# Kernel tuning notes

Measured on AMD Instinct MI355X. Metric: run time of the kernel, lower is better.

The kernel has to match this reference:

```python
import jax, jax.numpy as jnp
import numpy as np

NEG_SLOPE = 0.01   # F.leaky_relu default
EPS_NORM = 1e-12   # F.normalize default eps

N_NODES = 20000
N_RAND_EDGES = 320000
D_IN = 128
D_EMB = 128
C1 = 256
C2 = 32


def _segment_mean(vals, idx, n):
    s = jax.ops.segment_sum(vals, idx, num_segments=n)
    cnt = jax.ops.segment_sum(jnp.ones((vals.shape[0],), vals.dtype), idx, num_segments=n)
    return s / jnp.maximum(cnt, 1.0)[:, None]


def gcn_mean_sparse(h, W, b, src, dst, n):
    # GCN_layer with att=False: copy_u + mean over in-neighbors
    z = h @ W + b
    return _segment_mean(z[src], dst, n)


def gat_sparse(h, W, b, aW, ab, src, dst, n):
    # GCN_layer with att=True on an edge-list graph.
    # att_linear(cat(src,dst)) decomposed: e = leaky_relu(z_src@aWs + z_dst@aWd + ab)
    z = h @ W + b                       # [n, c]
    c = z.shape[-1]
    a_src = (z @ aW[:c])[:, 0]          # [n]
    a_dst = (z @ aW[c:])[:, 0]          # [n]
    e = jax.nn.leaky_relu(a_src[src] + a_dst[dst] + ab[0], NEG_SLOPE)  # [E]
    m = jax.ops.segment_max(e, dst, num_segments=n)                    # softmax over mailbox (per dst)
    alpha = jnp.exp(e - m[dst])
    denom = jax.ops.segment_sum(alpha, dst, num_segments=n)
    num = jax.ops.segment_sum(alpha[:, None] * z[src], dst, num_segments=n)  # [n, c]
    return num / denom[:, None]


def gat_dense(h, W, b, aW, ab):
    # att=True on a complete graph (coarse levels): dense softmax over src axis per dst
    z = h @ W + b                       # [n, c]
    c = z.shape[-1]
    a_src = z @ aW[:c]                  # [n, 1]
    a_dst = z @ aW[c:]                  # [n, 1]
    e = jax.nn.leaky_relu(a_src + a_dst.T + ab[0], NEG_SLOPE)  # [n_src, n_dst]
    alpha = jax.nn.softmax(e, axis=0)
    return jnp.einsum('ij,ic->jc', alpha, z)


def setup_inputs() -> dict:
    key = jax.random.key(0)
    ks = jax.random.split(key, 16)
    feature = jax.random.normal(ks[0], (N_NODES, D_IN), dtype=jnp.float32)
    src = jax.random.randint(ks[1], (N_RAND_EDGES,), 0, N_NODES, dtype=jnp.int32)
    dst = jax.random.randint(ks[2], (N_RAND_EDGES,), 0, N_NODES, dtype=jnp.int32)
    loop = jnp.arange(N_NODES, dtype=jnp.int32)
    edge_index = jnp.stack([jnp.concatenate([src, loop]), jnp.concatenate([dst, loop])])

    def lin(k, fan_in, fan_out):
        s = 1.0 / np.sqrt(fan_in)
        kw, kb = jax.random.split(k)
        W = jax.random.uniform(kw, (fan_in, fan_out), jnp.float32, -s, s)
        b = jax.random.uniform(kb, (fan_out,), jnp.float32, -s, s)
        return W, b

    Wf, bf = lin(ks[3], D_IN, D_EMB)          # GCN_f1
    We1, be1 = lin(ks[4], D_EMB, D_EMB)       # assign layer 1: GCN_emb
    Wa1, ba1 = lin(ks[5], D_EMB, C1)          # assign layer 1: GCN_ass linear
    attW1, attb1 = lin(ks[6], 2 * C1, 1)      # assign layer 1: att_linear
    We2, be2 = lin(ks[7], D_EMB, D_EMB)       # assign layer 2: GCN_emb
    Wa2, ba2 = lin(ks[8], D_EMB, C2)          # assign layer 2: GCN_ass linear
    attW2, attb2 = lin(ks[9], 2 * C2, 1)      # assign layer 2: att_linear
    return dict(feature=feature, edge_index=edge_index,
                Wf=Wf, bf=bf, We1=We1, be1=be1, Wa1=Wa1, ba1=ba1,
                attW1=attW1, attb1=attb1, We2=We2, be2=be2, Wa2=Wa2,
                ba2=ba2, attW2=attW2, attb2=attb2)


def reference(feature, edge_index, Wf, bf, We1, be1, Wa1, ba1, attW1, attb1,
              We2, be2, Wa2, ba2, attW2, attb2):
    src, dst = edge_index[0], edge_index[1]
    n = feature.shape[0]
    # GCN_f1 (att=False) + L2 normalize
    x = gcn_mean_sparse(feature, Wf, bf, src, dst, n)
    x = x / jnp.maximum(jnp.linalg.norm(x, axis=-1, keepdims=True), EPS_NORM)
    embed3 = x                                           # tree_node_embed[3]
    # Assign layer 1 (on original sparse graph)
    z1 = gcn_mean_sparse(x, We1, be1, src, dst, n)       # GCN_emb
    s1 = jax.nn.softmax(gat_sparse(z1, Wa1, ba1, attW1, attb1, src, dst, n), axis=-1)
    x1 = s1.T @ z1                                       # tree_node_embed[2], [C1, D]
    # Coarse graph: s^T A s with strictly positive softmax s -> complete graph
    # (setdiag(0) then add_self_loop => all pairs incl. self loops)
    # Assign layer 2 (dense complete graph over C1 nodes)
    lin2 = x1 @ We2 + be2
    z2 = jnp.broadcast_to(jnp.mean(lin2, axis=0, keepdims=True), lin2.shape)  # mean over all in-neighbors
    s2 = jax.nn.softmax(gat_dense(z2, Wa2, ba2, attW2, attb2), axis=-1)
    x2 = s2.T @ z2                                       # tree_node_embed[1], [C2, D]
    embed0 = jnp.mean(x2)                                # tree_node_embed[0] (scalar mean of all elems)
    assign1 = jnp.ones((s2.shape[-1], 1), dtype=x2.dtype)  # assignmatrix[1]
    # (assignmatrix[3], assignmatrix[2], assignmatrix[1], embed[3], embed[2], embed[1], embed[0])
    return (s1, s2, assign1, embed3, x1, x2, embed0)
```

## Files before the change

### kernel.cpp

```cpp
#include <hip/hip_runtime.h>
#include <hip/hip_bf16.h>
#include <math.h>

#define NN 20000
#define DD 128
#define CC1 256
#define CC2 32
#define X1_SPLIT 128

__device__ __forceinline__ unsigned short f2bf(float f) {
    unsigned int b = __float_as_uint(f);
    b = (b + 0x7fffu + ((b >> 16) & 1u)) >> 16;
    return (unsigned short)b;
}
__device__ __forceinline__ float bf_lo(unsigned int u) { return __uint_as_float(u << 16); }
__device__ __forceinline__ float bf_hi(unsigned int u) { return __uint_as_float(u & 0xffff0000u); }

__global__ void k_count(const int* __restrict__ dst, int* __restrict__ cnt, int E) {
    int e = blockIdx.x * blockDim.x + threadIdx.x;
    if (e < E) atomicAdd(&cnt[dst[e]], 1);
}

__global__ void k_scan(const int* __restrict__ cnt, int* __restrict__ offs, int n) {
    __shared__ int part[1024];
    int t = threadIdx.x;
    int chunk = (n + 1023) / 1024;
    int lo = t * chunk, hi = min(lo + chunk, n);
    int s = 0;
    for (int i = lo; i < hi; i++) s += cnt[i];
    part[t] = s;
    __syncthreads();
    for (int d = 1; d < 1024; d <<= 1) {
        int v = (t >= d) ? part[t - d] : 0;
        __syncthreads();
        part[t] += v;
        __syncthreads();
    }
    int base = (t > 0) ? part[t - 1] : 0;
    for (int i = lo; i < hi; i++) { offs[i] = base; base += cnt[i]; }
    if (t == 1023) offs[n] = part[1023];
}

__global__ void k_fill(const int* __restrict__ src, const int* __restrict__ dst,
                       const int* __restrict__ offs, int* __restrict__ fill,
                       int* __restrict__ csr_src, int E) {
    int e = blockIdx.x * blockDim.x + threadIdx.x;
    if (e < E) {
        int d = dst[e];
        int pos = atomicAdd(&fill[d], 1);
        csr_src[offs[d] + pos] = src[e];
    }
}

__global__ void k_fold(const float* __restrict__ Wa1, const float* __restrict__ ba1,
                       const float* __restrict__ attW1, const float* __restrict__ attb1,
                       float* __restrict__ fold) {
    int t = threadIdx.x;
    float vs = 0.f, vd = 0.f;
    for (int k = 0; k < CC1; k++) {
        float w = Wa1[t * CC1 + k];
        vs += w * attW1[k];
        vd += w * attW1[CC1 + k];
    }
    fold[t] = vs;
    fold[128 + t] = vd;
    if (t == 0) {
        float c = attb1[0];
        for (int k = 0; k < CC1; k++) c += ba1[k] * (attW1[k] + attW1[CC1 + k]);
        fold[256] = c;
    }
}

__global__ __launch_bounds__(256) void k_seg_mean(const float* __restrict__ in,
                                                  const int* __restrict__ offs,
                                                  const int* __restrict__ csr_src,
                                                  float* __restrict__ out, int n) {
    int wave = (blockIdx.x * blockDim.x + threadIdx.x) >> 6;
    int lane = threadIdx.x & 63;
    if (wave >= n) return;
    int lo = offs[wave], hi = offs[wave + 1];
    int half = lane >> 5, l32 = lane & 31;
    const float4* f4 = (const float4*)in;
    float4 acc = make_float4(0.f, 0.f, 0.f, 0.f);
    int i = lo + half;
    int sN = (i < hi) ? csr_src[i] : 0;
    while (i < hi) {
        int s = sN;
        int nx = i + 2;
        if (nx < hi) sN = csr_src[nx];
        float4 v = f4[(size_t)s * 32 + l32];
        acc.x += v.x; acc.y += v.y; acc.z += v.z; acc.w += v.w;
        i = nx;
    }
    acc.x += __shfl_xor(acc.x, 32);
    acc.y += __shfl_xor(acc.y, 32);
    acc.z += __shfl_xor(acc.z, 32);
    acc.w += __shfl_xor(acc.w, 32);
    if (half == 0) {
        float inv = 1.0f / (float)max(hi - lo, 1);
        float4 r = make_float4(acc.x * inv, acc.y * inv, acc.z * inv, acc.w * inv);
        ((float4*)out)[(size_t)wave * 32 + l32] = r;
    }
}

template <int MODE>
__global__ __launch_bounds__(256) void k_gemm128(const float* __restrict__ in,
                                                 const float* __restrict__ W,
                                                 const float* __restrict__ b,
                                                 float* __restrict__ out,
                                                 const float* __restrict__ fold,
                                                 float* __restrict__ a_src,
                                                 float* __restrict__ a_dst,
                                                 int n, int rows_per_block) {
    __shared__ float sW[128 * 128];
    __shared__ float sT[128][32];
    int t = threadIdx.x;
    for (int i = t; i < 128 * 128; i += 256) sW[i] = W[i];
    int lane = t & 63;
    int wv = t >> 6;
    int j4 = (lane & 31) * 4;
    int rh = lane >> 5;
    int rg = wv * 2 + rh;
    float bj0 = b[j4], bj1 = b[j4 + 1], bj2 = b[j4 + 2], bj3 = b[j4 + 3];
    float vs0 = 0.f, vs1 = 0.f, vs2 = 0.f, vs3 = 0.f;
    float vd0 = 0.f, vd1 = 0.f, vd2 = 0.f, vd3 = 0.f;
    if (MODE == 1) {
        vs0 = fold[j4]; vs1 = fold[j4 + 1]; vs2 = fold[j4 + 2]; vs3 = fold[j4 + 3];
        vd0 = fold[128 + j4]; vd1 = fold[128 + j4 + 1]; vd2 = fold[128 + j4 + 2]; vd3 = fold[128 + j4 + 3];
    }
    int row0 = blockIdx.x * rows_per_block;
    int row_end = min(row0 + rows_per_block, n);
    for (int r = row0; r < row_end; r += 32) {
        int nr = min(32, row_end - r);
        __syncthreads();
        {
            int lrow = t >> 3, seg = t & 7;
            if (lrow < nr) {
                const float4* g = (const float4*)&in[(size_t)(r + lrow) * 128 + seg * 16];
                float4 v0 = g[0], v1 = g[1], v2 = g[2], v3 = g[3];
                int k0 = seg * 16;
                sT[k0 + 0][lrow] = v0.x; sT[k0 + 1][lrow] = v0.y; sT[k0 + 2][lrow] = v0.z; sT[k0 + 3][lrow] = v0.w;
                sT[k0 + 4][lrow] = v1.x; sT[k0 + 5][lrow] = v1.y; sT[k0 + 6][lrow] = v1.z; sT[k0 + 7][lrow] = v1.w;
                sT[k0 + 8][lrow] = v2.x; sT[k0 + 9][lrow] = v2.y; sT[k0 + 10][lrow] = v2.z; sT[k0 + 11][lrow] = v2.w;
                sT[k0 + 12][lrow] = v3.x; sT[k0 + 13][lrow] = v3.y; sT[k0 + 14][lrow] = v3.z; sT[k0 + 15][lrow] = v3.w;
            }
        }
        __syncthreads();
        float acc[4][4];
        #pragma unroll
        for (int p = 0; p < 4; p++) { acc[p][0] = bj0; acc[p][1] = bj1; acc[p][2] = bj2; acc[p][3] = bj3; }
        for (int k = 0; k < 128; k++) {
            float4 w4 = *(const float4*)&sW[k * 128 + j4];
            float4 rv = *(const float4*)&sT[k][rg * 4];
            acc[0][0] += rv.x * w4.x; acc[0][1] += rv.x * w4.y; acc[0][2] += rv.x * w4.z; acc[0][3] += rv.x * w4.w;
            acc[1][0] += rv.y * w4.x; acc[1][1] += rv.y * w4.y; acc[1][2] += rv.y * w4.z; acc[1][3] += rv.y * w4.w;
            acc[2][0] += rv.z * w4.x; acc[2][1] += rv.z * w4.y; acc[2][2] += rv.z * w4.z; acc[2][3] += rv.z * w4.w;
            acc[3][0] += rv.w * w4.x; acc[3][1] += rv.w * w4.y; acc[3][2] += rv.w * w4.z; acc[3][3] += rv.w * w4.w;
        }
        #pragma unroll
        for (int p = 0; p < 4; p++) {
            int row = r + rg * 4 + p;
            if (MODE == 0) {
                float ss_ = acc[p][0] * acc[p][0] + acc[p][1] * acc[p][1] +
                            acc[p][2] * acc[p][2] + acc[p][3] * acc[p][3];
                ss_ += __shfl_xor(ss_, 16); ss_ += __shfl_xor(ss_, 8);
                ss_ += __shfl_xor(ss_, 4);  ss_ += __shfl_xor(ss_, 2); ss_ += __shfl_xor(ss_, 1);
                if (row < row_end) {
                    float scale = 1.0f / fmaxf(sqrtf(ss_), 1e-12f);
                    float4 o = make_float4(acc[p][0] * scale, acc[p][1] * scale, acc[p][2] * scale, acc[p][3] * scale);
                    *(float4*)&out[(size_t)row * 128 + j4] = o;
                }
            } else {
                if (row < row_end) {
                    float4 o = make_float4(acc[p][0], acc[p][1], acc[p][2], acc[p][3]);
                    *(float4*)&out[(size_t)row * 128 + j4] = o;
                }
                float ps = acc[p][0] * vs0 + acc[p][1] * vs1 + acc[p][2] * vs2 + acc[p][3] * vs3;
                float pd = acc[p][0] * vd0 + acc[p][1] * vd1 + acc[p][2] * vd2 + acc[p][3] * vd3;
                ps += __shfl_xor(ps, 16); ps += __shfl_xor(ps, 8); ps += __shfl_xor(ps, 4);
                ps += __shfl_xor(ps, 2);  ps += __shfl_xor(ps, 1);
                pd += __shfl_xor(pd, 16); pd += __shfl_xor(pd, 8); pd += __shfl_xor(pd, 4);
                pd += __shfl_xor(pd, 2);  pd += __shfl_xor(pd, 1);
                if (row < row_end && (lane & 31) == 0) {
                    a_src[row] = ps;
                    a_dst[row] = pd;
                }
            }
        }
    }
}

__global__ __launch_bounds__(256) void k_att(const float* __restrict__ z1,
                                             const int* __restrict__ offs,
                                             const int* __restrict__ csr_src,
                                             const float* __restrict__ a_src,
                                             const float* __restrict__ a_dst,
                                             const float* __restrict__ fold,
                                             float* __restrict__ r, int n) {
    int wave = (blockIdx.x * blockDim.x + threadIdx.x) >> 6;
    int lane = threadIdx.x & 63;
    if (wave >= n) return;
    int lo = offs[wave], hi = offs[wave + 1];
    float C0 = fold[256] + a_dst[wave];
    int half = lane >> 5, l32 = lane & 31;
    const float4* z4 = (const float4*)z1;
    float4 acc = make_float4(0.f, 0.f, 0.f, 0.f);
    float den = 0.f;
    int i = lo + half;
    int sN = (i < hi) ? csr_src[i] : 0;
    while (i < hi) {
        int s = sN;
        int nx = i + 2;
        if (nx < hi) sN = csr_src[nx];
        float a = a_src[s];
        float4 v = z4[(size_t)s * 32 + l32];
        float e = a + C0;
        e = e > 0.f ? e : 0.01f * e;
        e = fminf(e, 60.f);
        float al = __expf(e);
        den += al;
        acc.x += al * v.x; acc.y += al * v.y; acc.z += al * v.z; acc.w += al * v.w;
        i = nx;
    }
    den += __shfl_xor(den, 32);
    acc.x += __shfl_xor(acc.x, 32);
    acc.y += __shfl_xor(acc.y, 32);
    acc.z += __shfl_xor(acc.z, 32);
    acc.w += __shfl_xor(acc.w, 32);
    if (half == 0) {
        float invden = 1.0f / den;
        float4 o = make_float4(acc.x * invden, acc.y * invden, acc.z * invden, acc.w * invden);
        ((float4*)r)[(size_t)wave * 32 + l32] = o;
    }
}

__global__ __launch_bounds__(256) void k_s1(const float* __restrict__ r_,
                                            const float* __restrict__ Wa1,
                                            const float* __restrict__ ba1,
                                            float* __restrict__ s1, int n, int rows_per_block) {
    __shared__ unsigned short sW2[128 * 256];
    __shared__ float sT[128][32];
    int t = threadIdx.x;
    for (int i4 = t; i4 < 128 * 256 / 4; i4 += 256) {
        float4 v = ((const float4*)Wa1)[i4];
        ushort4 u;
        u.x = f2bf(v.x); u.y = f2bf(v.y); u.z = f2bf(v.z); u.w = f2bf(v.w);
        *(ushort4*)&sW2[i4 * 4] = u;
    }
    int cg = t & 31;
    int rg = t >> 5;
    int j8 = cg * 8;
    float bj[8];
    #pragma unroll
    for (int q = 0; q < 8; q++) bj[q] = ba1[j8 + q];
    int row0 = blockIdx.x * rows_per_block;
    int row_end = min(row0 + rows_per_block, n);
    for (int r = row0; r < row_end; r += 32) {
        int nr = min(32, row_end - r);
        __syncthreads();
        {
            int lrow = t >> 3, seg = t & 7;
            if (lrow < nr) {
                const float4* g = (const float4*)&r_[(size_t)(r + lrow) * 128 + seg * 16];
                float4 v0 = g[0], v1 = g[1], v2 = g[2], v3 = g[3];
                int k0 = seg * 16;
                sT[k0 + 0][lrow] = v0.x; sT[k0 + 1][lrow] = v0.y; sT[k0 + 2][lrow] = v0.z; sT[k0 + 3][lrow] = v0.w;
                sT[k0 + 4][lrow] = v1.x; sT[k0 + 5][lrow] = v1.y; sT[k0 + 6][lrow] = v1.z; sT[k0 + 7][lrow] = v1.w;
                sT[k0 + 8][lrow] = v2.x; sT[k0 + 9][lrow] = v2.y; sT[k0 + 10][lrow] = v2.z; sT[k0 + 11][lrow] = v2.w;
                sT[k0 + 12][lrow] = v3.x; sT[k0 + 13][lrow] = v3.y; sT[k0 + 14][lrow] = v3.z; sT[k0 + 15][lrow] = v3.w;
            }
        }
        __syncthreads();
        float acc[4][8];
        #pragma unroll
        for (int p = 0; p < 4; p++)
            #pragma unroll
            for (int q = 0; q < 8; q++) acc[p][q] = bj[q];
        for (int k = 0; k < 128; k++) {
            uint4 wz = *(const uint4*)&sW2[k * 256 + j8];
            float w0 = bf_lo(wz.x), w1 = bf_hi(wz.x), w2 = bf_lo(wz.y), w3 = bf_hi(wz.y);
            float w4 = bf_lo(wz.z), w5 = bf_hi(wz.z), w6 = bf_lo(wz.w), w7 = bf_hi(wz.w);
            float4 rv = *(const float4*)&sT[k][rg * 4];
            acc[0][0] += rv.x * w0; acc[0][1] += rv.x * w1; acc[0][2] += rv.x * w2; acc[0][3] += rv.x * w3;
            acc[0][4] += rv.x * w4; acc[0][5] += rv.x * w5; acc[0][6] += rv.x * w6; acc[0][7] += rv.x * w7;
            acc[1][0] += rv.y * w0; acc[1][1] += rv.y * w1; acc[1][2] += rv.y * w2; acc[1][3] += rv.y * w3;
            acc[1][4] += rv.y * w4; acc[1][5] += rv.y * w5; acc[1][6] += rv.y * w6; acc[1][7] += rv.y * w7;
            acc[2][0] += rv.z * w0; acc[2][1] += rv.z * w1; acc[2][2] += rv.z * w2; acc[2][3] += rv.z * w3;
            acc[2][4] += rv.z * w4; acc[2][5] += rv.z * w5; acc[2][6] += rv.z * w6; acc[2][7] += rv.z * w7;
            acc[3][0] += rv.w * w0; acc[3][1] += rv.w * w1; acc[3][2] += rv.w * w2; acc[3][3] += rv.w * w3;
            acc[3][4] += rv.w * w4; acc[3][5] += rv.w * w5; acc[3][6] += rv.w * w6; acc[3][7] += rv.w * w7;
        }
        #pragma unroll
        for (int p = 0; p < 4; p++) {
            int row = r + rg * 4 + p;
            float mx = acc[p][0];
            #pragma unroll
            for (int q = 1; q < 8; q++) mx = fmaxf(mx, acc[p][q]);
            mx = fmaxf(mx, __shfl_xor(mx, 16)); mx = fmaxf(mx, __shfl_xor(mx, 8));
            mx = fmaxf(mx, __shfl_xor(mx, 4));  mx = fmaxf(mx, __shfl_xor(mx, 2));
            mx = fmaxf(mx, __shfl_xor(mx, 1));
            float e[8], sm = 0.f;
            #pragma unroll
            for (int q = 0; q < 8; q++) { e[q] = __expf(acc[p][q] - mx); sm += e[q]; }
            sm += __shfl_xor(sm, 16); sm += __shfl_xor(sm, 8); sm += __shfl_xor(sm, 4);
            sm += __shfl_xor(sm, 2);  sm += __shfl_xor(sm, 1);
            if (row < row_end) {
                float inv = 1.0f / sm;
                float4 o0 = make_float4(e[0] * inv, e[1] * inv, e[2] * inv, e[3] * inv);
                float4 o1 = make_float4(e[4] * inv, e[5] * inv, e[6] * inv, e[7] * inv);
                *(float4*)&s1[(size_t)row * 256 + j8] = o0;
                *(float4*)&s1[(size_t)row * 256 + j8 + 4] = o1;
            }
        }
    }
}

__global__ __launch_bounds__(512) void k_x1(const float* __restrict__ s1,
                                            const float* __restrict__ z1,
                                            float* __restrict__ part, int n) {
    __shared__ float ss[16][128];
    __shared__ unsigned short sz[16][128];
    int t = threadIdx.x;
    int rs = blockIdx.x >> 1;
    int ch = blockIdx.x & 1;
    int c4 = (t & 31) * 4;
    int dg = t >> 5;
    int d0 = dg * 8;
    float a[4][8];
    #pragma unroll
    for (int c = 0; c < 4; c++)
        #pragma unroll
        for (int d = 0; d < 8; d++) a[c][d] = 0.f;
    int rows_per_block = (n + X1_SPLIT - 1) / X1_SPLIT;
    int row0 = rs * rows_per_block;
    int row_end = min(row0 + rows_per_block, n);
    int srow = t >> 5, scol4 = (t & 31) * 4;
    for (int r = row0; r < row_end; r += 16) {
        int nb = min(16, row_end - r);
        __syncthreads();
        if (srow < nb) {
            *(float4*)&ss[srow][scol4] = *(const float4*)&s1[(size_t)(r + srow) * 256 + ch * 128 + scol4];
            float4 zv = *(const float4*)&z1[(size_t)(r + srow) * 128 + scol4];
            ushort4 u;
            u.x = f2bf(zv.x); u.y = f2bf(zv.y); u.z = f2bf(zv.z); u.w = f2bf(zv.w);
            *(ushort4*)&sz[srow][scol4] = u;
        }
        __syncthreads();
        for (int i = 0; i < nb; i++) {
            float4 sv = *(const float4*)&ss[i][c4];
            uint4 zz = *(const uint4*)&sz[i][d0];
            float z0 = bf_lo(zz.x), z1f = bf_hi(zz.x), z2 = bf_lo(zz.y), z3 = bf_hi(zz.y);
            float z4 = bf_lo(zz.z), z5 = bf_hi(zz.z), z6 = bf_lo(zz.w), z7 = bf_hi(zz.w);
            float zf[8] = {z0, z1f, z2, z3, z4, z5, z6, z7};
            #pragma unroll
            for (int d = 0; d < 8; d++) {
                a[0][d] += sv.x * zf[d];
                a[1][d] += sv.y * zf[d];
                a[2][d] += sv.z * zf[d];
                a[3][d] += sv.w * zf[d];
            }
        }
    }
    size_t base = (size_t)rs * 32768 + (size_t)(ch * 128 + c4) * 128 + d0;
    #pragma unroll
    for (int c = 0; c < 4; c++) {
        *(float4*)&part[base + (size_t)c * 128]     = make_float4(a[c][0], a[c][1], a[c][2], a[c][3]);
        *(float4*)&part[base + (size_t)c * 128 + 4] = make_float4(a[c][4], a[c][5], a[c][6], a[c][7]);
    }
}

__global__ __launch_bounds__(256) void k_xred(const float* __restrict__ part,
                                              float* __restrict__ x1) {
    int o = blockIdx.x * 256 + threadIdx.x;
    float s = 0.f;
    for (int p = 0; p < X1_SPLIT; p++) s += part[(size_t)p * 32768 + o];
    x1[o] = s;
}

__global__ __launch_bounds__(256) void k_lin2(const float* __restrict__ x1,
                                              const float* __restrict__ We2,
                                              const float* __restrict__ be2,
                                              float* __restrict__ lin2) {
    int half = threadIdx.x >> 7, j = threadIdx.x & 127;
    int row = blockIdx.x * 2 + half;
    __shared__ float sr[2][128];
    sr[half][j] = x1[row * 128 + j];
    __syncthreads();
    float acc = be2[j];
    #pragma unroll 8
    for (int k = 0; k < 128; k++) acc += sr[half][k] * We2[k * 128 + j];
    lin2[row * 128 + j] = acc;
}

__global__ void k_coarse(const float* __restrict__ lin2, const float* __restrict__ Wa2,
                         const float* __restrict__ ba2,
                         float* __restrict__ s2, float* __restrict__ assign1,
                         float* __restrict__ x2, float* __restrict__ embed0) {
    __shared__ float mrow[128];
    __shared__ float p[32];
    __shared__ float red[2];
    int t = threadIdx.x;
    float s = 0.f;
    for (int i = 0; i < 256; i++) s += lin2[i * 128 + t];
    mrow[t] = s / 256.0f;
    __syncthreads();
    if (t < 32) {
        float z = ba2[t];
        for (int d = 0; d < 128; d++) z += mrow[d] * Wa2[d * 32 + t];
        float mx = z;
        for (int o = 16; o > 0; o >>= 1) mx = fmaxf(mx, __shfl_xor(mx, o, 32));
        float ex = __expf(z - mx);
        float sm = ex;
        for (int o = 16; o > 0; o >>= 1) sm += __shfl_xor(sm, o, 32);
        p[t] = ex / sm;
        assign1[t] = 1.0f;
    }
    __syncthreads();
    for (int i = t; i < 256 * 32; i += 128) s2[i] = p[i & 31];
    for (int i = t; i < 32 * 128; i += 128) {
        int k = i >> 7, d = i & 127;
        x2[i] = 256.0f * p[k] * mrow[d];
    }
    float tot = 0.f;
    for (int i = t; i < 32 * 128; i += 128) {
        int k = i >> 7, d = i & 127;
        tot += 256.0f * p[k] * mrow[d];
    }
    for (int o = 32; o > 0; o >>= 1) tot += __shfl_xor(tot, o);
    if ((t & 63) == 0) red[t >> 6] = tot;
    __syncthreads();
    if (t == 0) embed0[0] = (red[0] + red[1]) / 4096.0f;
}

extern "C" void kernel_launch(void* const* d_in, const int* in_sizes, int n_in,
                              void* d_out, int out_size, void* d_ws, size_t ws_size,
                              hipStream_t stream) {
    const float* feature = (const float*)d_in[0];
    const int*   eidx    = (const int*)d_in[1];
    const float* Wf   = (const float*)d_in[2];
    const float* bf   = (const float*)d_in[3];
    const float* We1  = (const float*)d_in[4];
    const float* be1  = (const float*)d_in[5];
    const float* Wa1  = (const float*)d_in[6];
    const float* ba1  = (const float*)d_in[7];
    const float* attW1= (const float*)d_in[8];
    const float* attb1= (const float*)d_in[9];
    const float* We2  = (const float*)d_in[10];
    const float* be2  = (const float*)d_in[11];
    const float* Wa2  = (const float*)d_in[12];
    const float* ba2  = (const float*)d_in[13];

    const int N = in_sizes[0] / DD;
    const int E = in_sizes[1] / 2;
    const int* src = eidx;
    const int* dst = eidx + E;

    float* out = (float*)d_out;
    float* s1_o      = out;
    float* s2_o      = s1_o + (size_t)N * CC1;
    float* assign1_o = s2_o + CC1 * CC2;
    float* embed3_o  = assign1_o + CC2;
    float* x1_o      = embed3_o + (size_t)N * DD;
    float* x2_o      = x1_o + CC1 * DD;
    float* embed0_o  = x2_o + CC2 * DD;

    char* w = (char*)d_ws;
    auto alloc = [&](size_t bytes) { void* p = (void*)w; w += ((bytes + 255) / 256) * 256; return p; };
    int* cnt   = (int*)alloc((size_t)N * 4);
    int* fill  = (int*)alloc((size_t)N * 4);
    int* offs  = (int*)alloc((size_t)(N + 1) * 4);
    int* csr   = (int*)alloc((size_t)E * 4);
    float* fold = (float*)alloc(257 * 4);
    float* z1   = (float*)alloc((size_t)N * DD * 4);
    float* a_src = (float*)alloc((size_t)N * 4);
    float* a_dst = (float*)alloc((size_t)N * 4);
    float* lin2  = (float*)alloc((size_t)CC1 * DD * 4);
    size_t agg_bytes = (size_t)N * DD * 4;
    size_t part_bytes = (size_t)X1_SPLIT * CC1 * DD * 4;
    float* agg  = (float*)alloc(agg_bytes > part_bytes ? agg_bytes : part_bytes);
    float* part = agg;

    hipMemsetAsync(cnt, 0, ((size_t)N * 4 + 255) / 256 * 256 + (size_t)N * 4, stream);

    k_count<<<(E + 255) / 256, 256, 0, stream>>>(dst, cnt, E);
    k_scan<<<1, 1024, 0, stream>>>(cnt, offs, N);
    k_fill<<<(E + 255) / 256, 256, 0, stream>>>(src, dst, offs, fill, csr, E);
    k_fold<<<1, 128, 0, stream>>>(Wa1, ba1, attW1, attb1, fold);

    int segBlocks = (N + 3) / 4;
    k_seg_mean<<<segBlocks, 256, 0, stream>>>(feature, offs, csr, agg, N);
    k_gemm128<0><<<(N + 63) / 64, 256, 0, stream>>>(agg, Wf, bf, embed3_o, nullptr, nullptr, nullptr, N, 64);
    k_seg_mean<<<segBlocks, 256, 0, stream>>>(embed3_o, offs, csr, agg, N);
    k_gemm128<1><<<(N + 63) / 64, 256, 0, stream>>>(agg, We1, be1, z1, fold, a_src, a_dst, N, 64);
    k_att<<<segBlocks, 256, 0, stream>>>(z1, offs, csr, a_src, a_dst, fold, agg, N);
    k_s1<<<(N + 63) / 64, 256, 0, stream>>>(agg, Wa1, ba1, s1_o, N, 64);
    k_x1<<<2 * X1_SPLIT, 512, 0, stream>>>(s1_o, z1, part, N);
    k_xred<<<CC1 * DD / 256, 256, 0, stream>>>(part, x1_o);
    k_lin2<<<CC1 / 2, 256, 0, stream>>>(x1_o, We2, be2, lin2);
    k_coarse<<<1, 128, 0, stream>>>(lin2, Wa2, ba2, s2_o, assign1_o, x2_o, embed0_o);
}
```

Measured before the change: 381.2 us.

## Gather bf16 node features in sparse aggregations and shrink GEMM tiles

Stores the input features, embed3 and z1 as bf16 copies so the three edge-gather kernels (two mean aggregations and the attention aggregation) read half the bytes per neighbor, and unrolls their gather loops by four. The GEMM kernels now process one 32-row tile per block with an XOR-swizzled transposed shared-memory layout and drop bounds checks. The bf16 copy of Wa1 is produced once in a prep kernel instead of in every k_s1 block. The trade-off is lower precision in the aggregated features, an extra conversion pass over the input, and reliance on N being a multiple of 32.

```diff
diff --git a/kernel.cpp b/kernel.cpp
--- a/kernel.cpp
+++ b/kernel.cpp
@@ -13,6 +13,7 @@
     b = (b + 0x7fffu + ((b >> 16) & 1u)) >> 16;
     return (unsigned short)b;
 }
+__device__ __forceinline__ float bfu(unsigned short u) { return __uint_as_float((unsigned int)u << 16); }
 __device__ __forceinline__ float bf_lo(unsigned int u) { return __uint_as_float(u << 16); }
 __device__ __forceinline__ float bf_hi(unsigned int u) { return __uint_as_float(u & 0xffff0000u); }
 
@@ -50,6 +51,22 @@
         int pos = atomicAdd(&fill[d], 1);
         csr_src[offs[d] + pos] = src[e];
     }
+}
+
+__global__ __launch_bounds__(256) void k_prep(const float* __restrict__ feature,
+                                              const float* __restrict__ Wa1,
+                                              unsigned short* __restrict__ feat_bf,
+                                              unsigned short* __restrict__ Wa1b, int nf4) {
+    int i = blockIdx.x * 256 + threadIdx.x;
+    int tot = nf4 + 128 * 256 / 4;
+    if (i >= tot) return;
+    float4 v;
+    if (i < nf4) v = ((const float4*)feature)[i];
+    else         v = ((const float4*)Wa1)[i - nf4];
+    ushort4 u;
+    u.x = f2bf(v.x); u.y = f2bf(v.y); u.z = f2bf(v.z); u.w = f2bf(v.w);
+    if (i < nf4) ((ushort4*)feat_bf)[i] = u;
+    else         ((ushort4*)Wa1b)[i - nf4] = u;
 }
 
 __global__ void k_fold(const float* __restrict__ Wa1, const float* __restrict__ ba1,
@@ -71,26 +88,34 @@
     }
 }
 
-__global__ __launch_bounds__(256) void k_seg_mean(const float* __restrict__ in,
-                                                  const int* __restrict__ offs,
-                                                  const int* __restrict__ csr_src,
-                                                  float* __restrict__ out, int n) {
+__global__ __launch_bounds__(256) void k_seg_mean_bf(const unsigned short* __restrict__ in,
+                                                     const int* __restrict__ offs,
+                                                     const int* __restrict__ csr_src,
+                                                     float* __restrict__ out, int n) {
     int wave = (blockIdx.x * blockDim.x + threadIdx.x) >> 6;
     int lane = threadIdx.x & 63;
     if (wave >= n) return;
     int lo = offs[wave], hi = offs[wave + 1];
     int half = lane >> 5, l32 = lane & 31;
-    const float4* f4 = (const float4*)in;
+    const ushort4* f = (const ushort4*)in;
     float4 acc = make_float4(0.f, 0.f, 0.f, 0.f);
     int i = lo + half;
-    int sN = (i < hi) ? csr_src[i] : 0;
+    while (i + 6 < hi) {
+        int s0 = csr_src[i], s1v = csr_src[i + 2], s2 = csr_src[i + 4], s3 = csr_src[i + 6];
+        ushort4 v0 = f[(size_t)s0 * 32 + l32];
+        ushort4 v1 = f[(size_t)s1v * 32 + l32];
+        ushort4 v2 = f[(size_t)s2 * 32 + l32];
+        ushort4 v3 = f[(size_t)s3 * 32 + l32];
+        acc.x += bfu(v0.x) + bfu(v1.x) + bfu(v2.x) + bfu(v3.x);
+        acc.y += bfu(v0.y) + bfu(v1.y) + bfu(v2.y) + bfu(v3.y);
+        acc.z += bfu(v0.z) + bfu(v1.z) + bfu(v2.z) + bfu(v3.z);
+        acc.w += bfu(v0.w) + bfu(v1.w) + bfu(v2.w) + bfu(v3.w);
+        i += 8;
+    }
     while (i < hi) {
-        int s = sN;
-        int nx = i + 2;
-        if (nx < hi) sN = csr_src[nx];
-        float4 v = f4[(size_t)s * 32 + l32];
-        acc.x += v.x; acc.y += v.y; acc.z += v.z; acc.w += v.w;
-        i = nx;
+        ushort4 v = f[(size_t)csr_src[i] * 32 + l32];
+        acc.x += bfu(v.x); acc.y += bfu(v.y); acc.z += bfu(v.z); acc.w += bfu(v.w);
+        i += 2;
     }
     acc.x += __shfl_xor(acc.x, 32);
     acc.y += __shfl_xor(acc.y, 32);
@@ -108,19 +133,34 @@
                                                  const float* __restrict__ W,
                                                  const float* __restrict__ b,
                                                  float* __restrict__ out,
+                                                 unsigned short* __restrict__ out_bf,
                                                  const float* __restrict__ fold,
                                                  float* __restrict__ a_src,
-                                                 float* __restrict__ a_dst,
-                                                 int n, int rows_per_block) {
+                                                 float* __restrict__ a_dst, int n) {
     __shared__ float sW[128 * 128];
-    __shared__ float sT[128][32];
+    __shared__ float sT[128 * 32];
     int t = threadIdx.x;
-    for (int i = t; i < 128 * 128; i += 256) sW[i] = W[i];
+    for (int i = t; i < 4096; i += 256) ((float4*)sW)[i] = ((const float4*)W)[i];
+    int r0 = blockIdx.x * 32;
+    {
+        int lrow = t >> 3, seg = t & 7;
+        const float4* g = (const float4*)&in[(size_t)(r0 + lrow) * 128 + seg * 16];
+        float4 v0 = g[0], v1 = g[1], v2 = g[2], v3 = g[3];
+        int base = (((lrow >> 2) ^ seg) << 2) + (lrow & 3);
+        int k0 = seg * 16;
+        sT[(k0 + 0) * 32 + base] = v0.x; sT[(k0 + 1) * 32 + base] = v0.y;
+        sT[(k0 + 2) * 32 + base] = v0.z; sT[(k0 + 3) * 32 + base] = v0.w;
+        sT[(k0 + 4) * 32 + base] = v1.x; sT[(k0 + 5) * 32 + base] = v1.y;
+        sT[(k0 + 6) * 32 + base] = v1.z; sT[(k0 + 7) * 32 + base] = v1.w;
+        sT[(k0 + 8) * 32 + base] = v2.x; sT[(k0 + 9) * 32 + base] = v2.y;
+        sT[(k0 + 10) * 32 + base] = v2.z; sT[(k0 + 11) * 32 + base] = v2.w;
+        sT[(k0 + 12) * 32 + base] = v3.x; sT[(k0 + 13) * 32 + base] = v3.y;
+        sT[(k0 + 14) * 32 + base] = v3.z; sT[(k0 + 15) * 32 + base] = v3.w;
+    }
     int lane = t & 63;
     int wv = t >> 6;
     int j4 = (lane & 31) * 4;
-    int rh = lane >> 5;
-    int rg = wv * 2 + rh;
+    int rg = wv * 2 + (lane >> 5);
     float bj0 = b[j4], bj1 = b[j4 + 1], bj2 = b[j4 + 2], bj3 = b[j4 + 3];
     float vs0 = 0.f, vs1 = 0.f, vs2 = 0.f, vs3 = 0.f;
     float vd0 = 0.f, vd1 = 0.f, vd2 = 0.f, vd3 = 0.f;
@@ -128,69 +168,46 @@
         vs0 = fold[j4]; vs1 = fold[j4 + 1]; vs2 = fold[j4 + 2]; vs3 = fold[j4 + 3];
         vd0 = fold[128 + j4]; vd1 = fold[128 + j4 + 1]; vd2 = fold[128 + j4 + 2]; vd3 = fold[128 + j4 + 3];
     }
-    int row0 = blockIdx.x * rows_per_block;
-    int row_end = min(row0 + rows_per_block, n);
-    for (int r = row0; r < row_end; r += 32) {
-        int nr = min(32, row_end - r);
-        __syncthreads();
-        {
-            int lrow = t >> 3, seg = t & 7;
-            if (lrow < nr) {
-                const float4* g = (const float4*)&in[(size_t)(r + lrow) * 128 + seg * 16];
-                float4 v0 = g[0], v1 = g[1], v2 = g[2], v3 = g[3];
-                int k0 = seg * 16;
-                sT[k0 + 0][lrow] = v0.x; sT[k0 + 1][lrow] = v0.y; sT[k0 + 2][lrow] = v0.z; sT[k0 + 3][lrow] = v0.w;
-                sT[k0 + 4][lrow] = v1.x; sT[k0 + 5][lrow] = v1.y; sT[k0 + 6][lrow] = v1.z; sT[k0 + 7][lrow] = v1.w;
-                sT[k0 + 8][lrow] = v2.x; sT[k0 + 9][lrow] = v2.y; sT[k0 + 10][lrow] = v2.z; sT[k0 + 11][lrow] = v2.w;
-                sT[k0 + 12][lrow] = v3.x; sT[k0 + 13][lrow] = v3.y; sT[k0 + 14][lrow] = v3.z; sT[k0 + 15][lrow] = v3.w;
-            }
+    __syncthreads();
+    float acc[4][4];
+    #pragma unroll
+    for (int p = 0; p < 4; p++) { acc[p][0] = bj0; acc[p][1] = bj1; acc[p][2] = bj2; acc[p][3] = bj3; }
+    for (int k = 0; k < 128; k++) {
+        float4 w4 = *(const float4*)&sW[k * 128 + j4];
+        float4 rv = *(const float4*)&sT[k * 32 + ((rg ^ (k >> 4)) << 2)];
+        acc[0][0] += rv.x * w4.x; acc[0][1] += rv.x * w4.y; acc[0][2] += rv.x * w4.z; acc[0][3] += rv.x * w4.w;
+        acc[1][0] += rv.y * w4.x; acc[1][1] += rv.y * w4.y; acc[1][2] += rv.y * w4.z; acc[1][3] += rv.y * w4.w;
+        acc[2][0] += rv.z * w4.x; acc[2][1] += rv.z * w4.y; acc[2][2] += rv.z * w4.z; acc[2][3] += rv.z * w4.w;
+        acc[3][0] += rv.w * w4.x; acc[3][1] += rv.w * w4.y; acc[3][2] += rv.w * w4.z; acc[3][3] += rv.w * w4.w;
+    }
+    #pragma unroll
+    for (int p = 0; p < 4; p++) {
+        int row = r0 + rg * 4 + p;
+        if (MODE == 0) {
+            float ss_ = acc[p][0] * acc[p][0] + acc[p][1] * acc[p][1] +
+                        acc[p][2] * acc[p][2] + acc[p][3] * acc[p][3];
+            ss_ += __shfl_xor(ss_, 16); ss_ += __shfl_xor(ss_, 8);
+            ss_ += __shfl_xor(ss_, 4);  ss_ += __shfl_xor(ss_, 2); ss_ += __shfl_xor(ss_, 1);
+            float scale = 1.0f / fmaxf(sqrtf(ss_), 1e-12f);
+            float o0 = acc[p][0] * scale, o1 = acc[p][1] * scale, o2 = acc[p][2] * scale, o3 = acc[p][3] * scale;
+            *(float4*)&out[(size_t)row * 128 + j4] = make_float4(o0, o1, o2, o3);
+            ushort4 u; u.x = f2bf(o0); u.y = f2bf(o1); u.z = f2bf(o2); u.w = f2bf(o3);
+            ((ushort4*)out_bf)[(size_t)row * 32 + (j4 >> 2)] = u;
+        } else {
+            ushort4 u; u.x = f2bf(acc[p][0]); u.y = f2bf(acc[p][1]); u.z = f2bf(acc[p][2]); u.w = f2bf(acc[p][3]);
+            ((ushort4*)out_bf)[(size_t)row * 32 + (j4 >> 2)] = u;
+            float ps = acc[p][0] * vs0 + acc[p][1] * vs1 + acc[p][2] * vs2 + acc[p][3] * vs3;
+            float pd = acc[p][0] * vd0 + acc[p][1] * vd1 + acc[p][2] * vd2 + acc[p][3] * vd3;
+            ps += __shfl_xor(ps, 16); ps += __shfl_xor(ps, 8); ps += __shfl_xor(ps, 4);
+            ps += __shfl_xor(ps, 2);  ps += __shfl_xor(ps, 1);
+            pd += __shfl_xor(pd, 16); pd += __shfl_xor(pd, 8); pd += __shfl_xor(pd, 4);
+            pd += __shfl_xor(pd, 2);  pd += __shfl_xor(pd, 1);
+            if ((lane & 31) == 0) { a_src[row] = ps; a_dst[row] = pd; }
         }
-        __syncthreads();
-        float acc[4][4];
-        #pragma unroll
-        for (int p = 0; p < 4; p++) { acc[p][0] = bj0; acc[p][1] = bj1; acc[p][2] = bj2; acc[p][3] = bj3; }
-        for (int k = 0; k < 128; k++) {
-            float4 w4 = *(const float4*)&sW[k * 128 + j4];
-            float4 rv = *(const float4*)&sT[k][rg * 4];
-            acc[0][0] += rv.x * w4.x; acc[0][1] += rv.x * w4.y; acc[0][2] += rv.x * w4.z; acc[0][3] += rv.x * w4.w;
-            acc[1][0] += rv.y * w4.x; acc[1][1] += rv.y * w4.y; acc[1][2] += rv.y * w4.z; acc[1][3] += rv.y * w4.w;
-            acc[2][0] += rv.z * w4.x; acc[2][1] += rv.z * w4.y; acc[2][2] += rv.z * w4.z; acc[2][3] += rv.z * w4.w;
-            acc[3][0] += rv.w * w4.x; acc[3][1] += rv.w * w4.y; acc[3][2] += rv.w * w4.z; acc[3][3] += rv.w * w4.w;
-        }
-        #pragma unroll
-        for (int p = 0; p < 4; p++) {
-            int row = r + rg * 4 + p;
-            if (MODE == 0) {
-                float ss_ = acc[p][0] * acc[p][0] + acc[p][1] * acc[p][1] +
-                            acc[p][2] * acc[p][2] + acc[p][3] * acc[p][3];
-                ss_ += __shfl_xor(ss_, 16); ss_ += __shfl_xor(ss_, 8);
-                ss_ += __shfl_xor(ss_, 4);  ss_ += __shfl_xor(ss_, 2); ss_ += __shfl_xor(ss_, 1);
-                if (row < row_end) {
-                    float scale = 1.0f / fmaxf(sqrtf(ss_), 1e-12f);
-                    float4 o = make_float4(acc[p][0] * scale, acc[p][1] * scale, acc[p][2] * scale, acc[p][3] * scale);
-                    *(float4*)&out[(size_t)row * 128 + j4] = o;
-                }
-            } else {
-                if (row < row_end) {
-                    float4 o = make_float4(acc[p][0], acc[p][1], acc[p][2], acc[p][3]);
-                    *(float4*)&out[(size_t)row * 128 + j4] = o;
-                }
-                float ps = acc[p][0] * vs0 + acc[p][1] * vs1 + acc[p][2] * vs2 + acc[p][3] * vs3;
-                float pd = acc[p][0] * vd0 + acc[p][1] * vd1 + acc[p][2] * vd2 + acc[p][3] * vd3;
-                ps += __shfl_xor(ps, 16); ps += __shfl_xor(ps, 8); ps += __shfl_xor(ps, 4);
-                ps += __shfl_xor(ps, 2);  ps += __shfl_xor(ps, 1);
-                pd += __shfl_xor(pd, 16); pd += __shfl_xor(pd, 8); pd += __shfl_xor(pd, 4);
-                pd += __shfl_xor(pd, 2);  pd += __shfl_xor(pd, 1);
-                if (row < row_end && (lane & 31) == 0) {
-                    a_src[row] = ps;
-                    a_dst[row] = pd;
-                }
-            }
-        }
-    }
-}
-
-__global__ __launch_bounds__(256) void k_att(const float* __restrict__ z1,
+    }
+}
+
+__global__ __launch_bounds__(256) void k_att(const unsigned short* __restrict__ z1b,
                                              const int* __restrict__ offs,
                                              const int* __restrict__ csr_src,
                                              const float* __restrict__ a_src,
@@ -203,24 +220,40 @@
     int lo = offs[wave], hi = offs[wave + 1];
     float C0 = fold[256] + a_dst[wave];
     int half = lane >> 5, l32 = lane & 31;
-    const float4* z4 = (const float4*)z1;
+    const ushort4* z4 = (const ushort4*)z1b;
     float4 acc = make_float4(0.f, 0.f, 0.f, 0.f);
     float den = 0.f;
     int i = lo + half;
-    int sN = (i < hi) ? csr_src[i] : 0;
+    while (i + 6 < hi) {
+        int s0 = csr_src[i], s1v = csr_src[i + 2], s2 = csr_src[i + 4], s3 = csr_src[i + 6];
+        float a0 = a_src[s0], a1 = a_src[s1v], a2 = a_src[s2], a3 = a_src[s3];
+        ushort4 v0 = z4[(size_t)s0 * 32 + l32];
+        ushort4 v1 = z4[(size_t)s1v * 32 + l32];
+        ushort4 v2 = z4[(size_t)s2 * 32 + l32];
+        ushort4 v3 = z4[(size_t)s3 * 32 + l32];
+        float e0 = a0 + C0; e0 = e0 > 0.f ? e0 : 0.01f * e0;
+        float e1 = a1 + C0; e1 = e1 > 0.f ? e1 : 0.01f * e1;
+        float e2 = a2 + C0; e2 = e2 > 0.f ? e2 : 0.01f * e2;
+        float e3 = a3 + C0; e3 = e3 > 0.f ? e3 : 0.01f * e3;
+        float al0 = __expf(fminf(e0, 60.f)), al1 = __expf(fminf(e1, 60.f));
+        float al2 = __expf(fminf(e2, 60.f)), al3 = __expf(fminf(e3, 60.f));
+        den += (al0 + al1) + (al2 + al3);
+        acc.x += al0 * bfu(v0.x) + al1 * bfu(v1.x) + al2 * bfu(v2.x) + al3 * bfu(v3.x);
+        acc.y += al0 * bfu(v0.y) + al1 * bfu(v1.y) + al2 * bfu(v2.y) + al3 * bfu(v3.y);
+        acc.z += al0 * bfu(v0.z) + al1 * bfu(v1.z) + al2 * bfu(v2.z) + al3 * bfu(v3.z);
+        acc.w += al0 * bfu(v0.w) + al1 * bfu(v1.w) + al2 * bfu(v2.w) + al3 * bfu(v3.w);
+        i += 8;
+    }
     while (i < hi) {
-        int s = sN;
-        int nx = i + 2;
-        if (nx < hi) sN = csr_src[nx];
+        int s = csr_src[i];
         float a = a_src[s];
-        float4 v = z4[(size_t)s * 32 + l32];
-        float e = a + C0;
-        e = e > 0.f ? e : 0.01f * e;
-        e = fminf(e, 60.f);
-        float al = __expf(e);
+        ushort4 v = z4[(size_t)s * 32 + l32];
+        float e = a + C0; e = e > 0.f ? e : 0.01f * e;
+        float al = __expf(fminf(e, 60.f));
         den += al;
-        acc.x += al * v.x; acc.y += al * v.y; acc.z += al * v.z; acc.w += al * v.w;
-        i = nx;
+        acc.x += al * bfu(v.x); acc.y += al * bfu(v.y);
+        acc.z += al * bfu(v.z); acc.w += al * bfu(v.w);
+        i += 2;
     }
     den += __shfl_xor(den, 32);
     acc.x += __shfl_xor(acc.x, 32);
@@ -235,88 +268,81 @@
 }
 
 __global__ __launch_bounds__(256) void k_s1(const float* __restrict__ r_,
-                                            const float* __restrict__ Wa1,
+                                            const unsigned short* __restrict__ Wa1b,
                                             const float* __restrict__ ba1,
-                                            float* __restrict__ s1, int n, int rows_per_block) {
+                                            float* __restrict__ s1, int n) {
     __shared__ unsigned short sW2[128 * 256];
-    __shared__ float sT[128][32];
+    __shared__ float sT[128 * 32];
     int t = threadIdx.x;
-    for (int i4 = t; i4 < 128 * 256 / 4; i4 += 256) {
-        float4 v = ((const float4*)Wa1)[i4];
-        ushort4 u;
-        u.x = f2bf(v.x); u.y = f2bf(v.y); u.z = f2bf(v.z); u.w = f2bf(v.w);
-        *(ushort4*)&sW2[i4 * 4] = u;
-    }
-    int cg = t & 31;
-    int rg = t >> 5;
+    {
+        const uint4* g = (const uint4*)Wa1b;
+        uint4* d = (uint4*)sW2;
+        #pragma unroll
+        for (int i = 0; i < 16; i++) d[t + i * 256] = g[t + i * 256];
+    }
+    int r0 = blockIdx.x * 32;
+    {
+        int lrow = t >> 3, seg = t & 7;
+        const float4* g = (const float4*)&r_[(size_t)(r0 + lrow) * 128 + seg * 16];
+        float4 v0 = g[0], v1 = g[1], v2 = g[2], v3 = g[3];
+        int base = (((lrow >> 2) ^ seg) << 2) + (lrow & 3);
+        int k0 = seg * 16;
+        sT[(k0 + 0) * 32 + base] = v0.x; sT[(k0 + 1) * 32 + base] = v0.y;
+        sT[(k0 + 2) * 32 + base] = v0.z; sT[(k0 + 3) * 32 + base] = v0.w;
+        sT[(k0 + 4) * 32 + base] = v1.x; sT[(k0 + 5) * 32 + base] = v1.y;
+        sT[(k0 + 6) * 32 + base] = v1.z; sT[(k0 + 7) * 32 + base] = v1.w;
+        sT[(k0 + 8) * 32 + base] = v2.x; sT[(k0 + 9) * 32 + base] = v2.y;
+        sT[(k0 + 10) * 32 + base] = v2.z; sT[(k0 + 11) * 32 + base] = v2.w;
+        sT[(k0 + 12) * 32 + base] = v3.x; sT[(k0 + 13) * 32 + base] = v3.y;
+        sT[(k0 + 14) * 32 + base] = v3.z; sT[(k0 + 15) * 32 + base] = v3.w;
+    }
+    int cg = t & 31, rg = t >> 5;
     int j8 = cg * 8;
     float bj[8];
     #pragma unroll
     for (int q = 0; q < 8; q++) bj[q] = ba1[j8 + q];
-    int row0 = blockIdx.x * rows_per_block;
-    int row_end = min(row0 + rows_per_block, n);
-    for (int r = row0; r < row_end; r += 32) {
-        int nr = min(32, row_end - r);
-        __syncthreads();
-        {
-            int lrow = t >> 3, seg = t & 7;
-            if (lrow < nr) {
-                const float4* g = (const float4*)&r_[(size_t)(r + lrow) * 128 + seg * 16];
-                float4 v0 = g[0], v1 = g[1], v2 = g[2], v3 = g[3];
-                int k0 = seg * 16;
-                sT[k0 + 0][lrow] = v0.x; sT[k0 + 1][lrow] = v0.y; sT[k0 + 2][lrow] = v0.z; sT[k0 + 3][lrow] = v0.w;
-                sT[k0 + 4][lrow] = v1.x; sT[k0 + 5][lrow] = v1.y; sT[k0 + 6][lrow] = v1.z; sT[k0 + 7][lrow] = v1.w;
-                sT[k0 + 8][lrow] = v2.x; sT[k0 + 9][lrow] = v2.y; sT[k0 + 10][lrow] = v2.z; sT[k0 + 11][lrow] = v2.w;
-                sT[k0 + 12][lrow] = v3.x; sT[k0 + 13][lrow] = v3.y; sT[k0 + 14][lrow] = v3.z; sT[k0 + 15][lrow] = v3.w;
-            }
-        }
-        __syncthreads();
-        float acc[4][8];
+    __syncthreads();
+    float acc[4][8];
+    #pragma unroll
+    for (int p = 0; p < 4; p++)
         #pragma unroll
-        for (int p = 0; p < 4; p++)
-            #pragma unroll
-            for (int q = 0; q < 8; q++) acc[p][q] = bj[q];
-        for (int k = 0; k < 128; k++) {
-            uint4 wz = *(const uint4*)&sW2[k * 256 + j8];
-            float w0 = bf_lo(wz.x), w1 = bf_hi(wz.x), w2 = bf_lo(wz.y), w3 = bf_hi(wz.y);
-            float w4 = bf_lo(wz.z), w5 = bf_hi(wz.z), w6 = bf_lo(wz.w), w7 = bf_hi(wz.w);
-            float4 rv = *(const float4*)&sT[k][rg * 4];
-            acc[0][0] += rv.x * w0; acc[0][1] += rv.x * w1; acc[0][2] += rv.x * w2; acc[0][3] += rv.x * w3;
-            acc[0][4] += rv.x * w4; acc[0][5] += rv.x * w5; acc[0][6] += rv.x * w6; acc[0][7] += rv.x * w7;
-            acc[1][0] += rv.y * w0; acc[1][1] += rv.y * w1; acc[1][2] += rv.y * w2; acc[1][3] += rv.y * w3;
-            acc[1][4] += rv.y * w4; acc[1][5] += rv.y * w5; acc[1][6] += rv.y * w6; acc[1][7] += rv.y * w7;
-            acc[2][0] += rv.z * w0; acc[2][1] += rv.z * w1; acc[2][2] += rv.z * w2; acc[2][3] += rv.z * w3;
-            acc[2][4] += rv.z * w4; acc[2][5] += rv.z * w5; acc[2][6] += rv.z * w6; acc[2][7] += rv.z * w7;
-            acc[3][0] += rv.w * w0; acc[3][1] += rv.w * w1; acc[3][2] += rv.w * w2; acc[3][3] += rv.w * w3;
-            acc[3][4] += rv.w * w4; acc[3][5] += rv.w * w5; acc[3][6] += rv.w * w6; acc[3][7] += rv.w * w7;
-        }
+        for (int q = 0; q < 8; q++) acc[p][q] = bj[q];
+    for (int k = 0; k < 128; k++) {
+        uint4 wz = *(const uint4*)&sW2[k * 256 + j8];
+        float w0 = bf_lo(wz.x), w1 = bf_hi(wz.x), w2 = bf_lo(wz.y), w3 = bf_hi(wz.y);
+        float w4 = bf_lo(wz.z), w5 = bf_hi(wz.z), w6 = bf_lo(wz.w), w7 = bf_hi(wz.w);
+        float4 rv = *(const float4*)&sT[k * 32 + ((rg ^ (k >> 4)) << 2)];
+        acc[0][0] += rv.x * w0; acc[0][1] += rv.x * w1; acc[0][2] += rv.x * w2; acc[0][3] += rv.x * w3;
+        acc[0][4] += rv.x * w4; acc[0][5] += rv.x * w5; acc[0][6] += rv.x * w6; acc[0][7] += rv.x * w7;
+        acc[1][0] += rv.y * w0; acc[1][1] += rv.y * w1; acc[1][2] += rv.y * w2; acc[1][3] += rv.y * w3;
+        acc[1][4] += rv.y * w4; acc[1][5] += rv.y * w5; acc[1][6] += rv.y * w6; acc[1][7] += rv.y * w7;
+        acc[2][0] += rv.z * w0; acc[2][1] += rv.z * w1; acc[2][2] += rv.z * w2; acc[2][3] += rv.z * w3;
+        acc[2][4] += rv.z * w4; acc[2][5] += rv.z * w5; acc[2][6] += rv.z * w6; acc[2][7] += rv.z * w7;
+        acc[3][0] += rv.w * w0; acc[3][1] += rv.w * w1; acc[3][2] += rv.w * w2; acc[3][3] += rv.w * w3;
+        acc[3][4] += rv.w * w4; acc[3][5] += rv.w * w5; acc[3][6] += rv.w * w6; acc[3][7] += rv.w * w7;
+    }
+    #pragma unroll
+    for (int p = 0; p < 4; p++) {
+        int row = r0 + rg * 4 + p;
+        float mx = acc[p][0];
         #pragma unroll
-        for (int p = 0; p < 4; p++) {
-            int row = r + rg * 4 + p;
-            float mx = acc[p][0];
-            #pragma unroll
-            for (int q = 1; q < 8; q++) mx = fmaxf(mx, acc[p][q]);
-            mx = fmaxf(mx, __shfl_xor(mx, 16)); mx = fmaxf(mx, __shfl_xor(mx, 8));
-            mx = fmaxf(mx, __shfl_xor(mx, 4));  mx = fmaxf(mx, __shfl_xor(mx, 2));
-            mx = fmaxf(mx, __shfl_xor(mx, 1));
-            float e[8], sm = 0.f;
-            #pragma unroll
-            for (int q = 0; q < 8; q++) { e[q] = __expf(acc[p][q] - mx); sm += e[q]; }
-            sm += __shfl_xor(sm, 16); sm += __shfl_xor(sm, 8); sm += __shfl_xor(sm, 4);
-            sm += __shfl_xor(sm, 2);  sm += __shfl_xor(sm, 1);
-            if (row < row_end) {
-                float inv = 1.0f / sm;
-                float4 o0 = make_float4(e[0] * inv, e[1] * inv, e[2] * inv, e[3] * inv);
-                float4 o1 = make_float4(e[4] * inv, e[5] * inv, e[6] * inv, e[7] * inv);
-                *(float4*)&s1[(size_t)row * 256 + j8] = o0;
-                *(float4*)&s1[(size_t)row * 256 + j8 + 4] = o1;
-            }
-        }
+        for (int q = 1; q < 8; q++) mx = fmaxf(mx, acc[p][q]);
+        mx = fmaxf(mx, __shfl_xor(mx, 16)); mx = fmaxf(mx, __shfl_xor(mx, 8));
+        mx = fmaxf(mx, __shfl_xor(mx, 4));  mx = fmaxf(mx, __shfl_xor(mx, 2));
+        mx = fmaxf(mx, __shfl_xor(mx, 1));
+        float e[8], sm = 0.f;
+        #pragma unroll
+        for (int q = 0; q < 8; q++) { e[q] = __expf(acc[p][q] - mx); sm += e[q]; }
+        sm += __shfl_xor(sm, 16); sm += __shfl_xor(sm, 8); sm += __shfl_xor(sm, 4);
+        sm += __shfl_xor(sm, 2);  sm += __shfl_xor(sm, 1);
+        float inv = 1.0f / sm;
+        *(float4*)&s1[(size_t)row * 256 + j8]     = make_float4(e[0] * inv, e[1] * inv, e[2] * inv, e[3] * inv);
+        *(float4*)&s1[(size_t)row * 256 + j8 + 4] = make_float4(e[4] * inv, e[5] * inv, e[6] * inv, e[7] * inv);
     }
 }
 
 __global__ __launch_bounds__(512) void k_x1(const float* __restrict__ s1,
-                                            const float* __restrict__ z1,
+                                            const unsigned short* __restrict__ z1b,
                                             float* __restrict__ part, int n) {
     __shared__ float ss[16][128];
     __shared__ unsigned short sz[16][128];
@@ -340,18 +366,15 @@
         __syncthreads();
         if (srow < nb) {
             *(float4*)&ss[srow][scol4] = *(const float4*)&s1[(size_t)(r + srow) * 256 + ch * 128 + scol4];
-            float4 zv = *(const float4*)&z1[(size_t)(r + srow) * 128 + scol4];
-            ushort4 u;
-            u.x = f2bf(zv.x); u.y = f2bf(zv.y); u.z = f2bf(zv.z); u.w = f2bf(zv.w);
-            *(ushort4*)&sz[srow][scol4] = u;
+            ((ushort4*)&sz[srow][0])[t & 31] = ((const ushort4*)z1b)[(size_t)(r + srow) * 32 + (t & 31)];
         }
         __syncthreads();
         for (int i = 0; i < nb; i++) {
             float4 sv = *(const float4*)&ss[i][c4];
             uint4 zz = *(const uint4*)&sz[i][d0];
-            float z0 = bf_lo(zz.x), z1f = bf_hi(zz.x), z2 = bf_lo(zz.y), z3 = bf_hi(zz.y);
-            float z4 = bf_lo(zz.z), z5 = bf_hi(zz.z), z6 = bf_lo(zz.w), z7 = bf_hi(zz.w);
-            float zf[8] = {z0, z1f, z2, z3, z4, z5, z6, z7};
+            float zf[8];
+            zf[0] = bf_lo(zz.x); zf[1] = bf_hi(zz.x); zf[2] = bf_lo(zz.y); zf[3] = bf_hi(zz.y);
+            zf[4] = bf_lo(zz.z); zf[5] = bf_hi(zz.z); zf[6] = bf_lo(zz.w); zf[7] = bf_hi(zz.w);
             #pragma unroll
             for (int d = 0; d < 8; d++) {
                 a[0][d] += sv.x * zf[d];
@@ -471,7 +494,10 @@
     int* offs  = (int*)alloc((size_t)(N + 1) * 4);
     int* csr   = (int*)alloc((size_t)E * 4);
     float* fold = (float*)alloc(257 * 4);
-    float* z1   = (float*)alloc((size_t)N * DD * 4);
+    unsigned short* feat_bf = (unsigned short*)alloc((size_t)N * DD * 2);
+    unsigned short* e3_bf   = (unsigned short*)alloc((size_t)N * DD * 2);
+    unsigned short* z1b     = (unsigned short*)alloc((size_t)N * DD * 2);
+    unsigned short* Wa1b    = (unsigned short*)alloc((size_t)128 * 256 * 2);
     float* a_src = (float*)alloc((size_t)N * 4);
     float* a_dst = (float*)alloc((size_t)N * 4);
     float* lin2  = (float*)alloc((size_t)CC1 * DD * 4);
@@ -485,16 +511,19 @@
     k_count<<<(E + 255) / 256, 256, 0, stream>>>(dst, cnt, E);
     k_scan<<<1, 1024, 0, stream>>>(cnt, offs, N);
     k_fill<<<(E + 255) / 256, 256, 0, stream>>>(src, dst, offs, fill, csr, E);
+    int nf4 = N * DD / 4;
+    k_prep<<<(nf4 + 128 * 256 / 4 + 255) / 256, 256, 0, stream>>>(feature, Wa1, feat_bf, Wa1b, nf4);
     k_fold<<<1, 128, 0, stream>>>(Wa1, ba1, attW1, attb1, fold);
 
     int segBlocks = (N + 3) / 4;
-    k_seg_mean<<<segBlocks, 256, 0, stream>>>(feature, offs, csr, agg, N);
-    k_gemm128<0><<<(N + 63) / 64, 256, 0, stream>>>(agg, Wf, bf, embed3_o, nullptr, nullptr, nullptr, N, 64);
-    k_seg_mean<<<segBlocks, 256, 0, stream>>>(embed3_o, offs, csr, agg, N);
-    k_gemm128<1><<<(N + 63) / 64, 256, 0, stream>>>(agg, We1, be1, z1, fold, a_src, a_dst, N, 64);
-    k_att<<<segBlocks, 256, 0, stream>>>(z1, offs, csr, a_src, a_dst, fold, agg, N);
-    k_s1<<<(N + 63) / 64, 256, 0, stream>>>(agg, Wa1, ba1, s1_o, N, 64);
-    k_x1<<<2 * X1_SPLIT, 512, 0, stream>>>(s1_o, z1, part, N);
+    int chunkBlocks = N / 32;
+    k_seg_mean_bf<<<segBlocks, 256, 0, stream>>>(feat_bf, offs, csr, agg, N);
+    k_gemm128<0><<<chunkBlocks, 256, 0, stream>>>(agg, Wf, bf, embed3_o, e3_bf, nullptr, nullptr, nullptr, N);
+    k_seg_mean_bf<<<segBlocks, 256, 0, stream>>>(e3_bf, offs, csr, agg, N);
+    k_gemm128<1><<<chunkBlocks, 256, 0, stream>>>(agg, We1, be1, nullptr, z1b, fold, a_src, a_dst, N);
+    k_att<<<segBlocks, 256, 0, stream>>>(z1b, offs, csr, a_src, a_dst, fold, agg, N);
+    k_s1<<<chunkBlocks, 256, 0, stream>>>(agg, Wa1b, ba1, s1_o, N);
+    k_x1<<<2 * X1_SPLIT, 512, 0, stream>>>(s1_o, z1b, part, N);
     k_xred<<<CC1 * DD / 256, 256, 0, stream>>>(part, x1_o);
     k_lin2<<<CC1 / 2, 256, 0, stream>>>(x1_o, We2, be2, lin2);
     k_coarse<<<1, 128, 0, stream>>>(lin2, Wa2, ba2, s2_o, assign1_o, x2_o, embed0_o);
```

Result: faster. 353.4 us (-7.3%).
